# Optimization experiments

Hardware: AMD Instinct MI355X
Metric: run time of the kernel (lower is better)

The kernel has to match this reference:

```python
import jax, jax.numpy as jnp
import numpy as np

B = 64
BAND = 16384
N_OSC = 32
CH = 64
T_IN = 32
N_NOISE_FRAMES = BAND // 4          # 4096
NOISE_STEP = BAND // N_NOISE_FRAMES  # 4 samples per noise frame
NOISE_COEFFS = NOISE_STEP // 2 + 1   # 3 rfft coefficients
N_UP = int(np.log2(N_NOISE_FRAMES) - np.log2(T_IN))  # 7 doubling blocks
LOWEST_FREQ = 20.0 / 11025.0


def _conv1d(x, w, b, pad):
    # x: (B, Cin, T), w: (Cout, Cin, K)
    out = jax.lax.conv_general_dilated(x, w, (1,), [(pad, pad)],
                                       dimension_numbers=('NCH', 'OIH', 'NCH'))
    return out + b[None, :, None]


def _leaky(x):
    return jnp.where(x > 0, x, 0.2 * x)


def _lin_interp(x, size):
    # torch F.interpolate(mode='linear', align_corners=False) along last axis
    n = x.shape[-1]
    coords = (jnp.arange(size, dtype=jnp.float32) + 0.5) * (n / size) - 0.5
    coords = jnp.clip(coords, 0.0, n - 1.0)
    lo = jnp.floor(coords).astype(jnp.int32)
    hi = jnp.minimum(lo + 1, n - 1)
    frac = (coords - lo.astype(jnp.float32)).astype(x.dtype)
    return x[..., lo] * (1.0 - frac) + x[..., hi] * frac


def setup_inputs() -> dict:
    key = jax.random.key(0)
    ks = jax.random.split(key, 16)
    s = 0.1
    return {
        'x': jax.random.normal(ks[0], (B, T_IN, CH), jnp.float32),
        'noise': jax.random.uniform(ks[1], (B, N_NOISE_FRAMES, NOISE_STEP), jnp.float32, -1.0, 1.0),
        'net_w': jax.random.normal(ks[2], (4, CH, CH, 3), jnp.float32) * s,
        'net_b': jax.random.normal(ks[3], (4, CH), jnp.float32) * s,
        'final_w': jax.random.normal(ks[4], (CH, CH, 3), jnp.float32) * s,
        'final_b': jax.random.normal(ks[5], (CH,), jnp.float32) * s,
        'amp_w': jax.random.normal(ks[6], (N_OSC, CH), jnp.float32) * s,
        'amp_b': jax.random.normal(ks[7], (N_OSC,), jnp.float32) * s,
        'freq_w': jax.random.normal(ks[8], (N_OSC, CH), jnp.float32) * s,
        'freq_b': jax.random.normal(ks[9], (N_OSC,), jnp.float32) * s,
        'nz_init_w': jax.random.normal(ks[10], (CH, CH), jnp.float32) * s,
        'nz_init_b': jax.random.normal(ks[11], (CH,), jnp.float32) * s,
        'nz_up_w': jax.random.normal(ks[12], (N_UP, CH, CH, 3), jnp.float32) * s,
        'nz_up_b': jax.random.normal(ks[13], (N_UP, CH), jnp.float32) * s,
        'nz_final_w': jax.random.normal(ks[14], (NOISE_COEFFS, CH), jnp.float32) * s,
        'nz_final_b': jax.random.normal(ks[15], (NOISE_COEFFS,), jnp.float32) * s,
    }


def reference(x, noise, net_w, net_b, final_w, final_b, amp_w, amp_b, freq_w, freq_b,
              nz_init_w, nz_init_b, nz_up_w, nz_up_b, nz_final_w, nz_final_b):
    z = jnp.transpose(x, (0, 2, 1))  # (B, CH, T_IN)
    for i in range(4):
        z = _leaky(_conv1d(z, net_w[i], net_b[i], 1))
    z = _conv1d(z, final_w, final_b, 1)

    # --- OscillatorBank: sigmoid freq (constrained), abs amp, linear upsample,
    # phase accumulation via cumsum, summed sinusoids ---
    amp = jnp.abs(jnp.einsum('bct,oc->bot', z, amp_w) + amp_b[None, :, None])
    freq = jax.nn.sigmoid(jnp.einsum('bct,oc->bot', z, freq_w) + freq_b[None, :, None])
    freq = LOWEST_FREQ + freq * (1.0 - LOWEST_FREQ)
    amp = _lin_interp(amp, BAND)    # (B, N_OSC, BAND)
    freq = _lin_interp(freq, BAND)  # (B, N_OSC, BAND)
    phase = jnp.cumsum(freq * jnp.pi, axis=-1)
    harm = jnp.sum(amp * jnp.sin(phase), axis=1, keepdims=True)  # (B, 1, BAND)

    # 1x1 conv to rfft coeffs, squared, applied per-frame to uniform noise ---
    y = jnp.einsum('bct,oc->bot', z, nz_init_w) + nz_init_b[None, :, None]
    for i in range(N_UP):
        y = jnp.repeat(y, 2, axis=-1)
        y = _leaky(_conv1d(y, nz_up_w[i], nz_up_b[i], 1))
    coeffs = jnp.einsum('bct,oc->bot', y, nz_final_w) + nz_final_b[None, :, None]
    coeffs = coeffs ** 2                      # squared=True, activation=identity
    coeffs = jnp.transpose(coeffs, (0, 2, 1))  # (B, frames, NOISE_COEFFS)
    spec = jnp.fft.rfft(noise, axis=-1, norm='ortho')   # (B, frames, NOISE_COEFFS)
    filt = spec * coeffs.astype(spec.dtype)
    nz = jnp.fft.irfft(filt, n=NOISE_STEP, axis=-1, norm='ortho')  # (B, frames, step)
    nz = nz.reshape(B, 1, BAND)

    return harm + nz
```

## Files before the change

### kernel.cpp

```cpp
#include <hip/hip_runtime.h>
#include <math.h>

#define LOWEST_FREQ_F 0.00181405895691609977f

typedef short bf16x8 __attribute__((ext_vector_type(8)));
typedef float f32x16 __attribute__((ext_vector_type(16)));

__device__ __forceinline__ float lrelu(float x) { return x > 0.f ? x : 0.2f * x; }
__device__ __forceinline__ float sin_rev(float fr) { return __builtin_amdgcn_sinf(fr); }
__device__ __forceinline__ float bf2f(unsigned short u) {
  union { unsigned int i; float f; } x; x.i = ((unsigned int)u) << 16; return x.f;
}
__device__ __forceinline__ unsigned short f2bf(float f) {
  union { float f; unsigned int i; } x; x.f = f;
  unsigned int r = x.i + 0x7FFFu + ((x.i >> 16) & 1u);
  return (unsigned short)(r >> 16);
}
__device__ __forceinline__ unsigned int pack2(float a, float b) {
  return (unsigned int)f2bf(a) | ((unsigned int)f2bf(b) << 16);
}

__global__ __launch_bounds__(256) void prep_kernel(
    const float* __restrict__ net_w, const float* __restrict__ fin_w,
    const float* __restrict__ amp_w, const float* __restrict__ frq_w,
    const float* __restrict__ nzi_w, const float* __restrict__ nzu_w,
    float* __restrict__ wtF4, float* __restrict__ awfwT,
    float* __restrict__ nzT, short* __restrict__ wfold)
{
  __shared__ __align__(16) float wls[12288];
  const int tid = threadIdx.x;
  const int bx  = blockIdx.x;

  if (bx < 7) {
    const float4* src = (const float4*)(nzu_w + bx * 12288);
    #pragma unroll
    for (int i = 0; i < 12; ++i)
      ((float4*)wls)[tid + i*256] = src[tid + i*256];
    __syncthreads();
    short* dst = wfold + bx * 16384;
    for (int i = 0; i < 64; ++i) {
      int q = i*256 + tid;
      int pd = q >> 12, co = (q >> 6) & 63, ci = q & 63;
      const float* wb = wls + co*192 + ci*3;
      float v;
      if      (pd == 0) v = wb[0];
      else if (pd == 1) v = wb[1] + wb[2];
      else if (pd == 2) v = wb[0] + wb[1];
      else              v = wb[2];
      dst[q] = (short)f2bf(v);
    }
  } else if (bx < 12) {
    int l = bx - 7;
    const float* s0 = (l < 4) ? (net_w + l * 12288) : fin_w;
    const float4* src = (const float4*)s0;
    #pragma unroll
    for (int i = 0; i < 12; ++i)
      ((float4*)wls)[tid + i*256] = src[tid + i*256];
    __syncthreads();
    float4* dst = ((float4*)wtF4) + l * 4096;
    for (int i = 0; i < 16; ++i) {
      int q = i*256 + tid;
      int ci = q >> 6, co = q & 63;
      const float* wb = wls + co*192 + ci*3;
      dst[q] = make_float4(wb[0], wb[1], wb[2], 0.f);
    }
  } else {
    #pragma unroll
    for (int i = 0; i < 2; ++i)
      ((float4*)wls)[tid + i*256] = ((const float4*)amp_w)[tid + i*256];
    #pragma unroll
    for (int i = 0; i < 2; ++i)
      ((float4*)(wls + 2048))[tid + i*256] = ((const float4*)frq_w)[tid + i*256];
    #pragma unroll
    for (int i = 0; i < 4; ++i)
      ((float4*)(wls + 4096))[tid + i*256] = ((const float4*)nzi_w)[tid + i*256];
    __syncthreads();
    for (int i = 0; i < 16; ++i) {
      int q = i*256 + tid;
      int c2 = q >> 7, rem = q & 127, o = rem >> 2, k = rem & 3;
      int c = c2*2 + (k >> 1);
      awfwT[q] = (k & 1) ? wls[2048 + o*64 + c] : wls[o*64 + c];
    }
    for (int i = 0; i < 16; ++i) {
      int q = i*256 + tid;
      int c = q >> 6, o = q & 63;
      nzT[q] = wls[4096 + o*64 + c];
    }
  }
}

template<int NT>
__device__ __forceinline__ void up_stage2(
    const short* bin, short* bout,
    const short* __restrict__ wf, const float* __restrict__ bias, int tid,
    int roff, int pairbase, int smin, int smax)
{
  const int L  = tid & 63;
  const int w  = tid >> 6;
  const int mt = w & 1;
  const int pg = w >> 1;

  bf16x8 Af[4][4];
  {
    const short* wb = wf + (mt*32 + (L & 31))*64 + ((L >> 5) << 3);
    #pragma unroll
    for (int pd = 0; pd < 4; ++pd)
      #pragma unroll
      for (int ks = 0; ks < 4; ++ks)
        Af[pd][ks] = *(const bf16x8*)(wb + pd*4096 + ks*16);
  }
  f32x16 binit;
  #pragma unroll
  for (int r = 0; r < 16; ++r)
    binit[r] = bias[mt*32 + (r & 3) + 8*(r >> 2) + 4*(L >> 5)];

  for (int n = pg; n < NT; n += 2) {
    int sl = n*32 + (L & 31);
    const short* bp = bin + (sl + roff)*72 + ((L >> 5) << 3);
    f32x16 Ce = binit, Co = binit;
    #pragma unroll
    for (int ks = 0; ks < 4; ++ks) {
      bf16x8 Bm = *(const bf16x8*)(bp + ks*16);
      bf16x8 B0 = *(const bf16x8*)(bp + 72 + ks*16);
      bf16x8 Bp = *(const bf16x8*)(bp + 144 + ks*16);
      Ce = __builtin_amdgcn_mfma_f32_32x32x16_bf16(Af[0][ks], Bm, Ce, 0, 0, 0);
      Ce = __builtin_amdgcn_mfma_f32_32x32x16_bf16(Af[1][ks], B0, Ce, 0, 0, 0);
      Co = __builtin_amdgcn_mfma_f32_32x32x16_bf16(Af[2][ks], B0, Co, 0, 0, 0);
      Co = __builtin_amdgcn_mfma_f32_32x32x16_bf16(Af[3][ks], Bp, Co, 0, 0, 0);
    }
    const int s0 = 2*(sl + pairbase);
    const bool we = (s0 >= smin)     && (s0 < smax);
    const bool wo = (s0 + 1 >= smin) && (s0 + 1 < smax);
    #pragma unroll
    for (int q4 = 0; q4 < 4; ++q4) {
      int co0 = mt*32 + 8*q4 + 4*(L >> 5);
      uint2 ve, vo;
      ve.x = pack2(lrelu(Ce[4*q4+0]), lrelu(Ce[4*q4+1]));
      ve.y = pack2(lrelu(Ce[4*q4+2]), lrelu(Ce[4*q4+3]));
      vo.x = pack2(lrelu(Co[4*q4+0]), lrelu(Co[4*q4+1]));
      vo.y = pack2(lrelu(Co[4*q4+2]), lrelu(Co[4*q4+3]));
      if (we) *(uint2*)&bout[(2*sl)*72 + co0]     = ve;
      if (wo) *(uint2*)&bout[(2*sl + 1)*72 + co0] = vo;
    }
  }
}

__device__ __forceinline__ void up_stage_coef(
    const short* bin, const short* __restrict__ wf,
    const float* __restrict__ bias, const float* __restrict__ wl4,
    float* __restrict__ cf, int tid)
{
  const int L  = tid & 63;
  const int w  = tid >> 6;
  const int mt = w & 1;
  const int pg = w >> 1;

  bf16x8 Af[4][4];
  {
    const short* wb = wf + (mt*32 + (L & 31))*64 + ((L >> 5) << 3);
    #pragma unroll
    for (int pd = 0; pd < 4; ++pd)
      #pragma unroll
      for (int ks = 0; ks < 4; ++ks)
        Af[pd][ks] = *(const bf16x8*)(wb + pd*4096 + ks*16);
  }
  f32x16 binit;
  #pragma unroll
  for (int r = 0; r < 16; ++r)
    binit[r] = bias[mt*32 + (r & 3) + 8*(r >> 2) + 4*(L >> 5)];

  for (int n = pg; n < 8; n += 2) {
    int sl = n*32 + (L & 31);
    const short* bp = bin + (sl + 1)*72 + ((L >> 5) << 3);
    f32x16 Ce = binit, Co = binit;
    #pragma unroll
    for (int ks = 0; ks < 4; ++ks) {
      bf16x8 Bm = *(const bf16x8*)(bp + ks*16);
      bf16x8 B0 = *(const bf16x8*)(bp + 72 + ks*16);
      bf16x8 Bp = *(const bf16x8*)(bp + 144 + ks*16);
      Ce = __builtin_amdgcn_mfma_f32_32x32x16_bf16(Af[0][ks], Bm, Ce, 0, 0, 0);
      Ce = __builtin_amdgcn_mfma_f32_32x32x16_bf16(Af[1][ks], B0, Ce, 0, 0, 0);
      Co = __builtin_amdgcn_mfma_f32_32x32x16_bf16(Af[2][ks], B0, Co, 0, 0, 0);
      Co = __builtin_amdgcn_mfma_f32_32x32x16_bf16(Af[3][ks], Bp, Co, 0, 0, 0);
    }
    float c0e = 0.f, c1e = 0.f, c2e = 0.f;
    float c0o = 0.f, c1o = 0.f, c2o = 0.f;
    #pragma unroll
    for (int r = 0; r < 16; ++r) {
      int ch = mt*32 + 8*(r >> 2) + 4*(L >> 5) + (r & 3);
      float4 w4 = *(const float4*)&wl4[ch*4];
      float ye = lrelu(Ce[r]);
      float yo = lrelu(Co[r]);
      c0e = fmaf(w4.x, ye, c0e); c1e = fmaf(w4.y, ye, c1e); c2e = fmaf(w4.z, ye, c2e);
      c0o = fmaf(w4.x, yo, c0o); c1o = fmaf(w4.y, yo, c1o); c2o = fmaf(w4.z, yo, c2o);
    }
    c0e += __shfl_xor(c0e, 32, 64); c1e += __shfl_xor(c1e, 32, 64);
    c2e += __shfl_xor(c2e, 32, 64); c0o += __shfl_xor(c0o, 32, 64);
    c1o += __shfl_xor(c1o, 32, 64); c2o += __shfl_xor(c2o, 32, 64);
    if (L < 32) {
      int fe = 2*sl, fo = fe + 1;
      cf[mt*1536 + fe]        = c0e; cf[mt*1536 + 512 + fe]  = c1e;
      cf[mt*1536 + 1024 + fe] = c2e;
      cf[mt*1536 + fo]        = c0o; cf[mt*1536 + 512 + fo]  = c1o;
      cf[mt*1536 + 1024 + fo] = c2o;
    }
  }
}

__global__ __launch_bounds__(256) void up345(
    const unsigned short* __restrict__ y0g,
    const short* __restrict__ wfold, const float* __restrict__ nzu_b,
    const float* __restrict__ nzf_w, const float* __restrict__ nzf_b,
    float* __restrict__ csq)
{
  __shared__ __align__(16) short arena[521 * 72];
  __shared__ float wl4[256];
  short* y0b = arena;
  short* y1b = arena + 34*72;
  short* y2b = arena + 69*72;
  short* s3  = arena + 135*72;
  short* s4  = arena + 201*72;
  short* s5  = arena + 329*72;
  short* s6  = arena;
  float* cf  = (float*)(arena + 329*72);

  const int b   = blockIdx.y;
  const int bx  = blockIdx.x;
  const int tid = threadIdx.x;

  if (tid < 64) {
    wl4[tid*4 + 0] = nzf_w[tid];
    wl4[tid*4 + 1] = nzf_w[64 + tid];
    wl4[tid*4 + 2] = nzf_w[128 + tid];
    wl4[tid*4 + 3] = 0.f;
  }
  for (int i = tid; i < 4689; i += 256) ((uint4*)arena)[i] = make_uint4(0,0,0,0);
  __syncthreads();

  const unsigned short* inb = y0g + (size_t)b * 32 * 64;
  for (int c = tid; c < 34*8; c += 256) {
    int row = c >> 3, pos = (c & 7) << 3;
    int g = 4*bx - 2 + row;
    if (g >= 0 && g < 32)
      *(bf16x8*)&y0b[row*72 + pos] = *(const bf16x8*)(inb + (size_t)g*64 + pos);
  }
  __syncthreads();

  int lo, hi;
  lo = 8*bx - 2;   hi = 8*bx + 18;
  up_stage2<1>(y0b, y1b, wfold + 0*16384, nzu_b + 0*64, tid,
               0, 4*bx - 1, lo < 0 ? 0 : lo, hi > 64 ? 64 : hi);
  __syncthreads();
  lo = 16*bx - 2;  hi = 16*bx + 33;
  up_stage2<1>(y1b, y2b, wfold + 1*16384, nzu_b + 1*64, tid,
               0, 8*bx - 1, lo < 0 ? 0 : lo, hi > 128 ? 128 : hi);
  __syncthreads();
  lo = 32*bx - 2;  hi = 32*bx + 64;
  up_stage2<2>(y2b, s3, wfold + 2*16384, nzu_b + 2*64, tid,
               0, 16*bx - 1, lo < 0 ? 0 : lo, hi > 256 ? 256 : hi);
  __syncthreads();
  lo = 64*bx - 2;  hi = 64*bx + 126;
  up_stage2<2>(s3, s4, wfold + 3*16384, nzu_b + 3*64, tid,
               0, 32*bx - 1, lo < 0 ? 0 : lo, hi > 512 ? 512 : hi);
  __syncthreads();
  lo = 128*bx - 2; hi = 128*bx + 190;
  up_stage2<3>(s4, s5, wfold + 4*16384, nzu_b + 4*64, tid,
               0, 64*bx - 1, lo < 0 ? 0 : lo, hi > 1024 ? 1024 : hi);
  __syncthreads();

  for (int i = tid; i < 2340; i += 256) ((uint4*)arena)[i] = make_uint4(0,0,0,0);
  __syncthreads();

  hi = 256*bx + 258;
  up_stage2<5>(s5, s6, wfold + 5*16384, nzu_b + 5*64, tid,
               0, 128*bx - 1, 0, hi > 2048 ? 2048 : hi);
  __syncthreads();

  up_stage_coef(s6, wfold + 6*16384, nzu_b + 6*64, wl4, cf, tid);
  __syncthreads();

  {
    float b0 = nzf_b[0], b1 = nzf_b[1], b2 = nzf_b[2];
    for (int i = tid; i < 512; i += 256) {
      float c0 = b0 + cf[i]        + cf[1536 + i];
      float c1 = b1 + cf[512 + i]  + cf[1536 + 512 + i];
      float c2 = b2 + cf[1024 + i] + cf[1536 + 1024 + i];
      size_t base = (size_t)b*4096 + 512*bx + i;
      csq[base]            = c0 * c0;
      csq[262144 + base]   = c1 * c1;
      csq[524288 + base]   = c2 * c2;
    }
  }
}

__device__ __forceinline__ void load_w8(float4* W, const float4* wp, int cc) {
  #pragma unroll
  for (int k = 0; k < 8; ++k) W[k] = wp[(cc*8 + k)*64];
}
__device__ __forceinline__ void load_z8(float* Z, const float* pa, int cc, int t0) {
  #pragma unroll
  for (int k = 0; k < 8; ++k) {
    const float* r = pa + (cc*8 + k)*36 + t0;
    float4 a = *(const float4*)r;
    float2 b2 = *(const float2*)(r + 4);
    Z[k*6+0] = a.x; Z[k*6+1] = a.y; Z[k*6+2] = a.z;
    Z[k*6+3] = a.w; Z[k*6+4] = b2.x; Z[k*6+5] = b2.y;
  }
}
__device__ __forceinline__ void fma8(float* acc, const float4* W, const float* Z) {
  #pragma unroll
  for (int k = 0; k < 8; ++k) {
    #pragma unroll
    for (int j = 0; j < 4; ++j) {
      acc[j] = fmaf(W[k].x, Z[k*6+j],   acc[j]);
      acc[j] = fmaf(W[k].y, Z[k*6+j+1], acc[j]);
      acc[j] = fmaf(W[k].z, Z[k*6+j+2], acc[j]);
    }
  }
}

__global__ __launch_bounds__(512, 2) void z_front(
    const float* __restrict__ x, const float* __restrict__ wtF4,
    const float* __restrict__ net_b, const float* __restrict__ fin_b,
    const float* __restrict__ awfwT, const float* __restrict__ amp_b,
    const float* __restrict__ frq_b,
    const float* __restrict__ nzT, const float* __restrict__ nzi_b,
    unsigned short* __restrict__ y0g, float* __restrict__ amp_o,
    float* __restrict__ frq_o, float* __restrict__ ph_o)
{
  __shared__ __align__(16) char arena[31104];
  float* za = (float*)arena;
  float* zb = (float*)(arena + 9216);
  float* zt = (float*)(arena + 18432);
  float* fl = (float*)(arena + 26880);

  const int b   = blockIdx.x;
  const int tid = threadIdx.x;
  const int co  = tid & 63;
  const int wv  = tid >> 6;

  for (int idx = tid; idx < 2048; idx += 512) {
    int t = idx >> 6, c = idx & 63;
    za[c*36 + t + 1] = x[b*2048 + idx];
  }
  if (tid < 64) {
    za[tid*36] = 0.f; za[tid*36 + 33] = 0.f;
    zb[tid*36] = 0.f; zb[tid*36 + 33] = 0.f;
  }
  __syncthreads();

  float* pa = za;
  float* pb = zb;
  for (int l = 0; l < 5; ++l) {
    {
      const int t0 = wv << 2;
      float bv = (l < 4) ? net_b[l*64 + co] : fin_b[co];
      float acc[4];
      #pragma unroll
      for (int j = 0; j < 4; ++j) acc[j] = bv;

      const float4* wp = ((const float4*)wtF4) + l*4096 + co;
      float4 wA[8], wB[8];
      float  zA[48], zB[48];
      load_w8(wA, wp, 0);
      load_z8(zA, pa, 0, t0);

      #pragma unroll
      for (int cc = 0; cc < 8; ++cc) {
        if (cc & 1) {
          if (cc < 7) { load_w8(wA, wp, cc + 1); load_z8(zA, pa, cc + 1, t0); }
          fma8(acc, wB, zB);
        } else {
          if (cc < 7) { load_w8(wB, wp, cc + 1); load_z8(zB, pa, cc + 1, t0); }
          fma8(acc, wA, zA);
        }
      }

      if (l < 4) {
        #pragma unroll
        for (int j = 0; j < 4; ++j)
          pb[co*36 + t0 + j + 1] = lrelu(acc[j]);
      } else {
        #pragma unroll
        for (int j = 0; j < 4; ++j) {
          int t = t0 + j;
          pb[co*36 + t] = acc[j];
          zt[t*66 + co] = acc[j];
        }
      }
    }
    __syncthreads();
    float* tp = pa; pa = pb; pb = tp;
  }
  const float* zf = pa;

  {
    const int q = wv;
    float bv0 = nzi_b[co];
    float acc[4];
    #pragma unroll
    for (int j = 0; j < 4; ++j) acc[j] = bv0;
    #pragma unroll 8
    for (int c = 0; c < 64; ++c) {
      float4 zv = *(const float4*)(zf + c*36 + (q << 2));
      float wvv = nzT[c*64 + co];
      acc[0] = fmaf(wvv, zv.x, acc[0]);
      acc[1] = fmaf(wvv, zv.y, acc[1]);
      acc[2] = fmaf(wvv, zv.z, acc[2]);
      acc[3] = fmaf(wvv, zv.w, acc[3]);
    }
    unsigned short* yb = y0g + (size_t)b * 2048;
    #pragma unroll
    for (int j = 0; j < 4; ++j)
      yb[((q << 2) + j)*64 + co] = f2bf(acc[j]);
  }

  #pragma unroll
  for (int tt = 0; tt < 2; ++tt) {
    int task = tid + 512*tt;
    int o = task & 31, t = task >> 5;
    float aa = amp_b[o], ff = frq_b[o];
    #pragma unroll 8
    for (int c2 = 0; c2 < 32; ++c2) {
      float4 w4 = ((const float4*)awfwT)[c2*32 + o];
      float2 zv = *(const float2*)(zt + t*66 + c2*2);
      aa = fmaf(w4.x, zv.x, aa); ff = fmaf(w4.y, zv.x, ff);
      aa = fmaf(w4.z, zv.y, aa); ff = fmaf(w4.w, zv.y, ff);
    }
    aa = fabsf(aa);
    float sg = 1.f / (1.f + expf(-ff));
    float fq = LOWEST_FREQ_F + sg * (1.f - LOWEST_FREQ_F);
    amp_o[b*1024 + o*32 + t] = aa;
    frq_o[b*1024 + o*32 + t] = fq;
    fl[o*33 + t] = fq;
  }
  __syncthreads();

  if (wv == 7 && (tid & 63) < 32) {
    const int o = tid & 31;
    double P = 256.0 * (double)fl[o*33];
    double hd = P * 0.5;
    ph_o[b*1024 + o*32] = (float)(hd - floor(hd));
    for (int i = 1; i < 32; ++i) {
      P += 256.0 * ((double)fl[o*33 + i - 1] + (double)fl[o*33 + i]);
      hd = P * 0.5;
      ph_o[b*1024 + o*32 + i] = (float)(hd - floor(hd));
    }
  }
}

__global__ __launch_bounds__(256) void osc_noise(
    const float* __restrict__ csq,
    const float* __restrict__ noise,
    const float* __restrict__ amp, const float* __restrict__ frq,
    const float* __restrict__ ph, float* __restrict__ out)
{
  __shared__ float al[1024], fqv[1024], pl[1024];

  const int b   = blockIdx.y;
  const int tid = threadIdx.x;
  const int fb  = blockIdx.x * 256 + tid;

  for (int i = tid; i < 1024; i += 256) {
    al[i]  = amp[b*1024 + i];
    fqv[i] = frq[b*1024 + i];
    pl[i]  = ph[b*1024 + i];
  }
  __syncthreads();

  const size_t base = (size_t)b*4096 + fb;
  float c0 = csq[base];
  float c1 = csq[262144 + base];
  float c2 = csq[524288 + base];

  const float4 n = *(const float4*)(noise + base*4);
  float F0  = c0 * (n.x + n.y + n.z + n.w) * 0.5f;
  float F1r = c1 * (n.x - n.z) * 0.5f;
  float F1i = -(c1 * (n.y - n.w) * 0.5f);
  float F2  = c2 * (n.x - n.y + n.z - n.w) * 0.5f;
  float r0 = 0.5f * (F0 + 2.f*F1r + F2);
  float r1 = 0.5f * (F0 - 2.f*F1i - F2);
  float r2 = 0.5f * (F0 - 2.f*F1r + F2);
  float r3 = 0.5f * (F0 + 2.f*F1i - F2);

  const int t0 = fb * 4;
  float s0a = 0.f, s1a = 0.f, s2a = 0.f, s3a = 0.f;
  if (t0 < 256) {
    const float tp = (float)(t0 + 1) * 0.5f;
    #pragma unroll 4
    for (int o = 0; o < 32; ++o) {
      float f0 = fqv[o*32], am = al[o*32];
      float hf = 0.5f * f0;
      float v0 = tp * f0, v1 = v0 + hf, v2 = v1 + hf, v3 = v2 + hf;
      s0a += am * sin_rev(v0 - floorf(v0));
      s1a += am * sin_rev(v1 - floorf(v1));
      s2a += am * sin_rev(v2 - floorf(v2));
      s3a += am * sin_rev(v3 - floorf(v3));
    }
  } else if (t0 >= 16128) {
    const float tp = (float)(t0 - 16127) * 0.5f;
    #pragma unroll 4
    for (int o = 0; o < 32; ++o) {
      float f0 = fqv[o*32 + 31], am = al[o*32 + 31], p = pl[o*32 + 31];
      float hf = 0.5f * f0;
      float v0 = p + tp * f0, v1 = v0 + hf, v2 = v1 + hf, v3 = v2 + hf;
      s0a += am * sin_rev(v0 - floorf(v0));
      s1a += am * sin_rev(v1 - floorf(v1));
      s2a += am * sin_rev(v2 - floorf(v2));
      s3a += am * sin_rev(v3 - floorf(v3));
    }
  } else {
    const int i  = (t0 - 256) >> 9;
    const int m0 = (t0 - 256) & 511;
    float mm[4], fa[4], mq[4];
    #pragma unroll
    for (int js = 0; js < 4; ++js) {
      float mmv = (float)(m0 + 1 + js);
      mm[js] = mmv;
      fa[js] = ((float)(m0 + js) + 0.5f) * (1.f/512.f);
      mq[js] = mmv * mmv * (1.f/1024.f);
    }
    #pragma unroll 4
    for (int o = 0; o < 32; ++o) {
      float f0 = fqv[o*32 + i], f1 = fqv[o*32 + i + 1];
      float a0 = al[o*32 + i],  a1 = al[o*32 + i + 1];
      float p  = pl[o*32 + i];
      float df = f1 - f0, da = a1 - a0;
      #pragma unroll
      for (int js = 0; js < 4; ++js) {
        float av   = fmaf(da, fa[js], a0);
        float part = fmaf(df, mq[js], mm[js] * f0);
        float v    = fmaf(part, 0.5f, p);
        float fr   = v - floorf(v);
        float sv   = av * sin_rev(fr);
        if      (js == 0) s0a += sv;
        else if (js == 1) s1a += sv;
        else if (js == 2) s2a += sv;
        else              s3a += sv;
      }
    }
  }
  float4 res = make_float4(s0a + r0, s1a + r1, s2a + r2, s3a + r3);
  *(float4*)(out + base*4) = res;
}

extern "C" void kernel_launch(void* const* d_in, const int* in_sizes, int n_in,
                              void* d_out, int out_size, void* d_ws, size_t ws_size,
                              hipStream_t stream) {
  (void)in_sizes; (void)n_in; (void)out_size; (void)ws_size;
  const float* x     = (const float*)d_in[0];
  const float* noise = (const float*)d_in[1];
  const float* net_w = (const float*)d_in[2];
  const float* net_b = (const float*)d_in[3];
  const float* fin_w = (const float*)d_in[4];
  const float* fin_b = (const float*)d_in[5];
  const float* amp_w = (const float*)d_in[6];
  const float* amp_b = (const float*)d_in[7];
  const float* frq_w = (const float*)d_in[8];
  const float* frq_b = (const float*)d_in[9];
  const float* nzi_w = (const float*)d_in[10];
  const float* nzi_b = (const float*)d_in[11];
  const float* nzu_w = (const float*)d_in[12];
  const float* nzu_b = (const float*)d_in[13];
  const float* nzf_w = (const float*)d_in[14];
  const float* nzf_b = (const float*)d_in[15];
  float* out = (float*)d_out;

  short* y0    = (short*)d_ws;
  short* wfold = y0 + (size_t)64*32*64;
  float* wtF4  = (float*)(wfold + 7*16384);
  float* awfwT = wtF4 + 81920;
  float* nzT   = awfwT + 4096;
  float* ampv  = nzT + 4096;
  float* frqv  = ampv + 65536;
  float* phv   = frqv + 65536;
  float* csq   = phv + 65536;

  prep_kernel<<<dim3(13), dim3(256), 0, stream>>>(
      net_w, fin_w, amp_w, frq_w, nzi_w, nzu_w, wtF4, awfwT, nzT, wfold);

  z_front<<<dim3(64), dim3(512), 0, stream>>>(
      x, wtF4, net_b, fin_b, awfwT, amp_b, frq_b, nzT, nzi_b,
      (unsigned short*)y0, ampv, frqv, phv);

  up345<<<dim3(8, 64), dim3(256), 0, stream>>>(
      (unsigned short*)y0, wfold, nzu_b, nzf_w, nzf_b, csq);

  osc_noise<<<dim3(16, 64), dim3(256), 0, stream>>>(
      csq, noise, ampv, frqv, phv, out);
}
```

Measured before the change: 177.6 us.

## Fuse oscillator/noise synthesis into upsampling kernel with 512-thread blocks

Merges the separate osc_noise kernel into the upsampling kernel, so the squared noise coefficients stay in shared memory and are no longer written to and re-read from global memory. It also removes one kernel launch. Blocks grow from 256 to 512 threads and the MFMA stage loops now stride by 4 wave groups. The amp, freq and phase tables are loaded into the reused arena after the conv stages. The risk is that 512-thread blocks with a large LDS arena lower occupancy, and the synthesis now runs on only 512 blocks instead of 1024.

```diff
diff --git a/kernel.cpp b/kernel.cpp
--- a/kernel.cpp
+++ b/kernel.cpp
@@ -114,7 +114,7 @@
   for (int r = 0; r < 16; ++r)
     binit[r] = bias[mt*32 + (r & 3) + 8*(r >> 2) + 4*(L >> 5)];
 
-  for (int n = pg; n < NT; n += 2) {
+  for (int n = pg; n < NT; n += 4) {
     int sl = n*32 + (L & 31);
     const short* bp = bin + (sl + roff)*72 + ((L >> 5) << 3);
     f32x16 Ce = binit, Co = binit;
@@ -169,7 +169,7 @@
   for (int r = 0; r < 16; ++r)
     binit[r] = bias[mt*32 + (r & 3) + 8*(r >> 2) + 4*(L >> 5)];
 
-  for (int n = pg; n < 8; n += 2) {
+  for (int n = pg; n < 8; n += 4) {
     int sl = n*32 + (L & 31);
     const short* bp = bin + (sl + 1)*72 + ((L >> 5) << 3);
     f32x16 Ce = binit, Co = binit;
@@ -207,11 +207,13 @@
   }
 }
 
-__global__ __launch_bounds__(256) void up345(
+__global__ __launch_bounds__(512, 4) void up_osc(
     const unsigned short* __restrict__ y0g,
     const short* __restrict__ wfold, const float* __restrict__ nzu_b,
     const float* __restrict__ nzf_w, const float* __restrict__ nzf_b,
-    float* __restrict__ csq)
+    const float* __restrict__ noise,
+    const float* __restrict__ amp, const float* __restrict__ frq,
+    const float* __restrict__ ph, float* __restrict__ out)
 {
   __shared__ __align__(16) short arena[521 * 72];
   __shared__ float wl4[256];
@@ -223,6 +225,9 @@
   short* s5  = arena + 329*72;
   short* s6  = arena;
   float* cf  = (float*)(arena + 329*72);
+  float* al  = (float*)arena;
+  float* fqv = (float*)arena + 1024;
+  float* pl  = (float*)arena + 2048;
 
   const int b   = blockIdx.y;
   const int bx  = blockIdx.x;
@@ -234,11 +239,11 @@
     wl4[tid*4 + 2] = nzf_w[128 + tid];
     wl4[tid*4 + 3] = 0.f;
   }
-  for (int i = tid; i < 4689; i += 256) ((uint4*)arena)[i] = make_uint4(0,0,0,0);
+  for (int i = tid; i < 4689; i += 512) ((uint4*)arena)[i] = make_uint4(0,0,0,0);
   __syncthreads();
 
   const unsigned short* inb = y0g + (size_t)b * 32 * 64;
-  for (int c = tid; c < 34*8; c += 256) {
+  for (int c = tid; c < 34*8; c += 512) {
     int row = c >> 3, pos = (c & 7) << 3;
     int g = 4*bx - 2 + row;
     if (g >= 0 && g < 32)
@@ -268,7 +273,7 @@
                0, 64*bx - 1, lo < 0 ? 0 : lo, hi > 1024 ? 1024 : hi);
   __syncthreads();
 
-  for (int i = tid; i < 2340; i += 256) ((uint4*)arena)[i] = make_uint4(0,0,0,0);
+  for (int i = tid; i < 2340; i += 512) ((uint4*)arena)[i] = make_uint4(0,0,0,0);
   __syncthreads();
 
   hi = 256*bx + 258;
@@ -279,17 +284,90 @@
   up_stage_coef(s6, wfold + 6*16384, nzu_b + 6*64, wl4, cf, tid);
   __syncthreads();
 
+  for (int i = tid; i < 1024; i += 512) {
+    al[i]  = amp[b*1024 + i];
+    fqv[i] = frq[b*1024 + i];
+    pl[i]  = ph[b*1024 + i];
+  }
+  __syncthreads();
+
   {
-    float b0 = nzf_b[0], b1 = nzf_b[1], b2 = nzf_b[2];
-    for (int i = tid; i < 512; i += 256) {
-      float c0 = b0 + cf[i]        + cf[1536 + i];
-      float c1 = b1 + cf[512 + i]  + cf[1536 + 512 + i];
-      float c2 = b2 + cf[1024 + i] + cf[1536 + 1024 + i];
-      size_t base = (size_t)b*4096 + 512*bx + i;
-      csq[base]            = c0 * c0;
-      csq[262144 + base]   = c1 * c1;
-      csq[524288 + base]   = c2 * c2;
-    }
+    float c0 = nzf_b[0] + cf[tid]        + cf[1536 + tid];
+    float c1 = nzf_b[1] + cf[512 + tid]  + cf[1536 + 512 + tid];
+    float c2 = nzf_b[2] + cf[1024 + tid] + cf[1536 + 1024 + tid];
+    c0 *= c0; c1 *= c1; c2 *= c2;
+
+    const int fb = 512*bx + tid;
+    const size_t base = (size_t)b*4096 + fb;
+    const float4 n = *(const float4*)(noise + base*4);
+    float F0  = c0 * (n.x + n.y + n.z + n.w) * 0.5f;
+    float F1r = c1 * (n.x - n.z) * 0.5f;
+    float F1i = -(c1 * (n.y - n.w) * 0.5f);
+    float F2  = c2 * (n.x - n.y + n.z - n.w) * 0.5f;
+    float r0 = 0.5f * (F0 + 2.f*F1r + F2);
+    float r1 = 0.5f * (F0 - 2.f*F1i - F2);
+    float r2 = 0.5f * (F0 - 2.f*F1r + F2);
+    float r3 = 0.5f * (F0 + 2.f*F1i - F2);
+
+    const int t0 = fb * 4;
+    float s0a = 0.f, s1a = 0.f, s2a = 0.f, s3a = 0.f;
+    if (t0 < 256) {
+      const float tp = (float)(t0 + 1) * 0.5f;
+      #pragma unroll 4
+      for (int o = 0; o < 32; ++o) {
+        float f0 = fqv[o*32], am = al[o*32];
+        float hf = 0.5f * f0;
+        float v0 = tp * f0, v1 = v0 + hf, v2 = v1 + hf, v3 = v2 + hf;
+        s0a += am * sin_rev(v0 - floorf(v0));
+        s1a += am * sin_rev(v1 - floorf(v1));
+        s2a += am * sin_rev(v2 - floorf(v2));
+        s3a += am * sin_rev(v3 - floorf(v3));
+      }
+    } else if (t0 >= 16128) {
+      const float tp = (float)(t0 - 16127) * 0.5f;
+      #pragma unroll 4
+      for (int o = 0; o < 32; ++o) {
+        float f0 = fqv[o*32 + 31], am = al[o*32 + 31], p = pl[o*32 + 31];
+        float hf = 0.5f * f0;
+        float v0 = p + tp * f0, v1 = v0 + hf, v2 = v1 + hf, v3 = v2 + hf;
+        s0a += am * sin_rev(v0 - floorf(v0));
+        s1a += am * sin_rev(v1 - floorf(v1));
+        s2a += am * sin_rev(v2 - floorf(v2));
+        s3a += am * sin_rev(v3 - floorf(v3));
+      }
+    } else {
+      const int i  = (t0 - 256) >> 9;
+      const int m0 = (t0 - 256) & 511;
+      float mm[4], fa[4], mq[4];
+      #pragma unroll
+      for (int js = 0; js < 4; ++js) {
+        float mmv = (float)(m0 + 1 + js);
+        mm[js] = mmv;
+        fa[js] = ((float)(m0 + js) + 0.5f) * (1.f/512.f);
+        mq[js] = mmv * mmv * (1.f/1024.f);
+      }
+      #pragma unroll 4
+      for (int o = 0; o < 32; ++o) {
+        float f0 = fqv[o*32 + i], f1 = fqv[o*32 + i + 1];
+        float a0 = al[o*32 + i],  a1 = al[o*32 + i + 1];
+        float p  = pl[o*32 + i];
+        float df = f1 - f0, da = a1 - a0;
+        #pragma unroll
+        for (int js = 0; js < 4; ++js) {
+          float av   = fmaf(da, fa[js], a0);
+          float part = fmaf(df, mq[js], mm[js] * f0);
+          float v    = fmaf(part, 0.5f, p);
+          float fr   = v - floorf(v);
+          float sv   = av * sin_rev(fr);
+          if      (js == 0) s0a += sv;
+          else if (js == 1) s1a += sv;
+          else if (js == 2) s2a += sv;
+          else              s3a += sv;
+        }
+      }
+    }
+    float4 res = make_float4(s0a + r0, s1a + r1, s2a + r2, s3a + r3);
+    *(float4*)(out + base*4) = res;
   }
 }
 
@@ -447,101 +525,6 @@
       ph_o[b*1024 + o*32 + i] = (float)(hd - floor(hd));
     }
   }
-}
-
-__global__ __launch_bounds__(256) void osc_noise(
-    const float* __restrict__ csq,
-    const float* __restrict__ noise,
-    const float* __restrict__ amp, const float* __restrict__ frq,
-    const float* __restrict__ ph, float* __restrict__ out)
-{
-  __shared__ float al[1024], fqv[1024], pl[1024];
-
-  const int b   = blockIdx.y;
-  const int tid = threadIdx.x;
-  const int fb  = blockIdx.x * 256 + tid;
-
-  for (int i = tid; i < 1024; i += 256) {
-    al[i]  = amp[b*1024 + i];
-    fqv[i] = frq[b*1024 + i];
-    pl[i]  = ph[b*1024 + i];
-  }
-  __syncthreads();
-
-  const size_t base = (size_t)b*4096 + fb;
-  float c0 = csq[base];
-  float c1 = csq[262144 + base];
-  float c2 = csq[524288 + base];
-
-  const float4 n = *(const float4*)(noise + base*4);
-  float F0  = c0 * (n.x + n.y + n.z + n.w) * 0.5f;
-  float F1r = c1 * (n.x - n.z) * 0.5f;
-  float F1i = -(c1 * (n.y - n.w) * 0.5f);
-  float F2  = c2 * (n.x - n.y + n.z - n.w) * 0.5f;
-  float r0 = 0.5f * (F0 + 2.f*F1r + F2);
-  float r1 = 0.5f * (F0 - 2.f*F1i - F2);
-  float r2 = 0.5f * (F0 - 2.f*F1r + F2);
-  float r3 = 0.5f * (F0 + 2.f*F1i - F2);
-
-  const int t0 = fb * 4;
-  float s0a = 0.f, s1a = 0.f, s2a = 0.f, s3a = 0.f;
-  if (t0 < 256) {
-    const float tp = (float)(t0 + 1) * 0.5f;
-    #pragma unroll 4
-    for (int o = 0; o < 32; ++o) {
-      float f0 = fqv[o*32], am = al[o*32];
-      float hf = 0.5f * f0;
-      float v0 = tp * f0, v1 = v0 + hf, v2 = v1 + hf, v3 = v2 + hf;
-      s0a += am * sin_rev(v0 - floorf(v0));
-      s1a += am * sin_rev(v1 - floorf(v1));
-      s2a += am * sin_rev(v2 - floorf(v2));
-      s3a += am * sin_rev(v3 - floorf(v3));
-    }
-  } else if (t0 >= 16128) {
-    const float tp = (float)(t0 - 16127) * 0.5f;
-    #pragma unroll 4
-    for (int o = 0; o < 32; ++o) {
-      float f0 = fqv[o*32 + 31], am = al[o*32 + 31], p = pl[o*32 + 31];
-      float hf = 0.5f * f0;
-      float v0 = p + tp * f0, v1 = v0 + hf, v2 = v1 + hf, v3 = v2 + hf;
-      s0a += am * sin_rev(v0 - floorf(v0));
-      s1a += am * sin_rev(v1 - floorf(v1));
-      s2a += am * sin_rev(v2 - floorf(v2));
-      s3a += am * sin_rev(v3 - floorf(v3));
-    }
-  } else {
-    const int i  = (t0 - 256) >> 9;
-    const int m0 = (t0 - 256) & 511;
-    float mm[4], fa[4], mq[4];
-    #pragma unroll
-    for (int js = 0; js < 4; ++js) {
-      float mmv = (float)(m0 + 1 + js);
-      mm[js] = mmv;
-      fa[js] = ((float)(m0 + js) + 0.5f) * (1.f/512.f);
-      mq[js] = mmv * mmv * (1.f/1024.f);
-    }
-    #pragma unroll 4
-    for (int o = 0; o < 32; ++o) {
-      float f0 = fqv[o*32 + i], f1 = fqv[o*32 + i + 1];
-      float a0 = al[o*32 + i],  a1 = al[o*32 + i + 1];
-      float p  = pl[o*32 + i];
-      float df = f1 - f0, da = a1 - a0;
-      #pragma unroll
-      for (int js = 0; js < 4; ++js) {
-        float av   = fmaf(da, fa[js], a0);
-        float part = fmaf(df, mq[js], mm[js] * f0);
-        float v    = fmaf(part, 0.5f, p);
-        float fr   = v - floorf(v);
-        float sv   = av * sin_rev(fr);
-        if      (js == 0) s0a += sv;
-        else if (js == 1) s1a += sv;
-        else if (js == 2) s2a += sv;
-        else              s3a += sv;
-      }
-    }
-  }
-  float4 res = make_float4(s0a + r0, s1a + r1, s2a + r2, s3a + r3);
-  *(float4*)(out + base*4) = res;
 }
 
 extern "C" void kernel_launch(void* const* d_in, const int* in_sizes, int n_in,
@@ -574,7 +557,6 @@
   float* ampv  = nzT + 4096;
   float* frqv  = ampv + 65536;
   float* phv   = frqv + 65536;
-  float* csq   = phv + 65536;
 
   prep_kernel<<<dim3(13), dim3(256), 0, stream>>>(
       net_w, fin_w, amp_w, frq_w, nzi_w, nzu_w, wtF4, awfwT, nzT, wfold);
@@ -583,9 +565,7 @@
       x, wtF4, net_b, fin_b, awfwT, amp_b, frq_b, nzT, nzi_b,
       (unsigned short*)y0, ampv, frqv, phv);
 
-  up345<<<dim3(8, 64), dim3(256), 0, stream>>>(
-      (unsigned short*)y0, wfold, nzu_b, nzf_w, nzf_b, csq);
-
-  osc_noise<<<dim3(16, 64), dim3(256), 0, stream>>>(
-      csq, noise, ampv, frqv, phv, out);
-}
+  up_osc<<<dim3(8, 64), dim3(512), 0, stream>>>(
+      (unsigned short*)y0, wfold, nzu_b, nzf_w, nzf_b,
+      noise, ampv, frqv, phv, out);
+}
```

After: 232.5 us. 30.9% more time.
